# Kernel optimization log

Hardware: AMD Instinct MI355X
Metric: run time of the kernel (lower is better)

Reference implementation:

```python
import jax, jax.numpy as jnp
import numpy as np
from jax import lax

B, N, S, D1, D2 = 16, 4096, 1024, 128, 256
C_IN, C_MID, C_OUT = D1 + D2, 256, 128
BN_EPS = 1e-5


def setup_inputs() -> dict:
    key = jax.random.key(0)
    ks = jax.random.split(key, 12)
    return {
        "xyz1": jax.random.normal(ks[0], (B, N, 3), jnp.float32),
        "xyz2": jax.random.normal(ks[1], (B, S, 3), jnp.float32),
        "points1": jax.random.normal(ks[2], (B, N, D1), jnp.float32),
        "points2": jax.random.normal(ks[3], (B, S, D2), jnp.float32),
        # 1x1 Conv1d weights (kernel size 1 -> plain channel matmul)
        "W1": jax.random.normal(ks[4], (C_MID, C_IN), jnp.float32) * (1.0 / np.sqrt(C_IN)),
        "b1": jax.random.normal(ks[5], (C_MID,), jnp.float32) * 0.01,
        "g1": jnp.ones((C_MID,), jnp.float32),
        "be1": jnp.zeros((C_MID,), jnp.float32),
        "W2": jax.random.normal(ks[6], (C_OUT, C_MID), jnp.float32) * (1.0 / np.sqrt(C_MID)),
        "b2": jax.random.normal(ks[7], (C_OUT,), jnp.float32) * 0.01,
        "g2": jnp.ones((C_OUT,), jnp.float32),
        "be2": jnp.zeros((C_OUT,), jnp.float32),
    }


def _bn_relu(x, g, be):
    # BatchNorm1d in training mode: batch stats over (B, L) per channel, biased var
    mean = jnp.mean(x, axis=(0, 2), keepdims=True)
    var = jnp.var(x, axis=(0, 2), keepdims=True)
    y = (x - mean) * lax.rsqrt(var + BN_EPS)
    return jax.nn.relu(y * g[None, :, None] + be[None, :, None])


def reference(xyz1, xyz2, points1, points2, W1, b1, g1, be1, W2, b2, g2, be2):
    # squared pairwise distances [B,N,S] via ||a||^2 - 2ab + ||b||^2
    dist = (
        jnp.sum(xyz1 * xyz1, -1)[:, :, None]
        - 2.0 * jnp.einsum("bnd,bsd->bns", xyz1, xyz2)
        + jnp.sum(xyz2 * xyz2, -1)[:, None, :]
    )
    neg_d3, idx = lax.top_k(-dist, 3)            # 3 nearest neighbors
    d3 = -neg_d3                                  # [B,N,3]
    w = 1.0 / (d3 + 1e-8)
    w = w / jnp.sum(w, -1, keepdims=True)
    gathered = jax.vmap(lambda p, i: p[i])(points2, idx)   # [B,N,3,D2]
    interp = jnp.sum(gathered * w[..., None], axis=2)      # [B,N,D2]
    new_points = jnp.concatenate([points1, interp], axis=-1)  # [B,N,D1+D2]
    x = jnp.transpose(new_points, (0, 2, 1))                   # [B,C,N]
    x = _bn_relu(jnp.einsum("oc,bcn->bon", W1, x) + b1[None, :, None], g1, be1)
    x = _bn_relu(jnp.einsum("oc,bcn->bon", W2, x) + b2[None, :, None], g2, be2)
    return jnp.transpose(x, (0, 2, 1))                         # [B,N,C_OUT]
```

## Files before the change

### kernel.cpp

```cpp
#include <hip/hip_runtime.h>
#include <hip/hip_bf16.h>

#define NB    16
#define NPT   4096
#define NSRC  1024
#define ND1   128
#define ND2   256
#define NCIN  384
#define NCMID 256
#define NCOUT 128
#define BNTOT (NB * NPT)
#define BN_EPS 1e-5f

typedef float f32x4 __attribute__((ext_vector_type(4)));
typedef short bf16x8 __attribute__((ext_vector_type(8)));
typedef unsigned int uint;

union PK8 { unsigned short u[8]; uint4 q; };
union PK4 { unsigned short u[4]; uint2 q; };

static __device__ __forceinline__ unsigned short f2bf(float f) {
  __hip_bfloat16 h = __float2bfloat16(f);
  return __builtin_bit_cast(unsigned short, h);
}
static __device__ __forceinline__ float bf2f(unsigned short u) {
  return __builtin_bit_cast(float, (uint)u << 16);
}
static __device__ __forceinline__ void gl_lds16(const unsigned short* g, unsigned short* l) {
  __builtin_amdgcn_global_load_lds(
      (const __attribute__((address_space(1))) uint*)(const void*)g,
      (__attribute__((address_space(3))) uint*)(void*)l,
      16, 0, 0);
}

#if __has_builtin(__builtin_amdgcn_fmed3f)
#define MED3F(a, b, c) __builtin_amdgcn_fmed3f((a), (b), (c))
#else
#define MED3F(a, b, c) fmaxf((a), fminf((b), (c)))
#endif

static __device__ __forceinline__ bool prec(float da, int ia, float db, int ib) {
  return (da < db) || (da == db && ia < ib);
}

#define INSV(t0, t1, t2, j0, j1, j2, d, idx)                                   \
  {                                                                            \
    const bool c0 = (d) < t0;                                                  \
    const bool c1 = (d) < t1;                                                  \
    const bool c2 = (d) < t2;                                                  \
    const float m1 = MED3F(t0, t1, (d));                                       \
    const float m2 = fminf(t2, fmaxf(t1, (d)));                                \
    t0 = fminf(t0, (d));                                                       \
    j2 = c2 ? (c1 ? j1 : (idx)) : j2;                                          \
    j1 = c1 ? (c0 ? j0 : (idx)) : j1;                                          \
    j0 = c0 ? (idx) : j0;                                                      \
    t1 = m1; t2 = m2;                                                          \
  }

#define MERGE3(d0, j0, d1, j1, d2, j2, e0, i0, e1, i1, e2, i2)                 \
  {                                                                            \
    const bool p0 = prec(d0, j0, e0, i0);                                      \
    const float l0d = p0 ? e0 : d0; const int l0j = p0 ? i0 : j0;              \
    const float r0d = p0 ? d0 : e0; const int r0j = p0 ? j0 : i0;              \
    const bool p1 = prec(d1, j1, e1, i1);                                      \
    const float w1d = p1 ? d1 : e1; const int w1j = p1 ? j1 : i1;              \
    const bool pr1 = prec(l0d, l0j, w1d, w1j);                                 \
    const float r1d = pr1 ? l0d : w1d; const int r1j = pr1 ? l0j : w1j;        \
    const float q1d = pr1 ? w1d : l0d; const int q1j = pr1 ? w1j : l0j;        \
    const bool p2 = prec(d2, j2, e2, i2);                                      \
    const float w2d = p2 ? d2 : e2; const int w2j = p2 ? j2 : i2;              \
    const bool pr2 = prec(q1d, q1j, w2d, w2j);                                 \
    const float r2d = pr2 ? q1d : w2d; const int r2j = pr2 ? q1j : w2j;        \
    d0 = r0d; j0 = r0j; d1 = r1d; j1 = r1j; d2 = r2d; j2 = r2j;                \
  }

__global__ __launch_bounds__(256) void prep_w_kernel(
    const float* __restrict__ w1, const float* __restrict__ w2,
    unsigned short* __restrict__ w1b, unsigned short* __restrict__ w2b)
{
  const int i = blockIdx.x * 256 + threadIdx.x;
  const bool isW1 = i < 24576;
  const float4 v = isW1 ? ((const float4*)w1)[i] : ((const float4*)w2)[i - 24576];
  PK4 pk;
  pk.u[0] = f2bf(v.x); pk.u[1] = f2bf(v.y); pk.u[2] = f2bf(v.z); pk.u[3] = f2bf(v.w);
  if (isW1) ((uint2*)w1b)[i] = pk.q;
  else      ((uint2*)w2b)[i - 24576] = pk.q;
}

__global__ __launch_bounds__(512, 4) void fg1_kernel(
    const float* __restrict__ xyz1, const float* __restrict__ xyz2,
    const float* __restrict__ points1, const float* __restrict__ points2,
    const unsigned short* __restrict__ W1bf, const float* __restrict__ bias1,
    unsigned short* __restrict__ h1bf, float* __restrict__ sum1, float* __restrict__ sq1)
{
  __shared__ unsigned short sA[2][128][32];
  __shared__ unsigned short sB[2][256][32];
  __shared__ float4 s2t[4 * 257];
  __shared__ int   sj[128][3];
  __shared__ float sw[128][3];

  const int tid = threadIdx.x;
  const int lane = tid & 63;
  const int wave = tid >> 6;
  const int ptBase = blockIdx.x * 128;
  const int b = ptBase >> 12;

  const int fr = lane & 15;
  const int cs = lane >> 4;
  const int rdsh = ((cs ^ ((fr >> 1) & 3)) << 3);

  auto stageB = [&](int buf, int kt) {
    const int k0 = kt * 32;
#pragma unroll
    for (int c = 0; c < 2; ++c) {
      const int base = c * 512 + wave * 64;
      const int s = base + lane;
      const int row = s >> 2, c16 = s & 3;
      const int ks = c16 ^ ((row >> 1) & 3);
      gl_lds16(W1bf + (size_t)row * NCIN + k0 + ks * 8,
               &sB[buf][0][0] + base * 8);
    }
  };

  auto stageA = [&](int buf, int kt) {
    const int k0 = kt * 32;
    const int row = tid >> 2, c16 = tid & 3;
    const int ks = c16 ^ ((row >> 1) & 3);
    const int k = k0 + ks * 8;
    PK8 pk;
    if (k < ND1) {
      const float* src = points1 + (size_t)(ptBase + row) * ND1 + k;
      const float4 va = ((const float4*)src)[0];
      const float4 vb = ((const float4*)src)[1];
      pk.u[0] = f2bf(va.x); pk.u[1] = f2bf(va.y); pk.u[2] = f2bf(va.z); pk.u[3] = f2bf(va.w);
      pk.u[4] = f2bf(vb.x); pk.u[5] = f2bf(vb.y); pk.u[6] = f2bf(vb.z); pk.u[7] = f2bf(vb.w);
    } else {
      const float* p2 = points2 + (size_t)b * NSRC * ND2 + (k - ND1);
      const int j0 = sj[row][0], j1 = sj[row][1], j2 = sj[row][2];
      const float w0 = sw[row][0], w1 = sw[row][1], w2 = sw[row][2];
      const float4* r0 = (const float4*)(p2 + (size_t)j0 * ND2);
      const float4* r1 = (const float4*)(p2 + (size_t)j1 * ND2);
      const float4* r2 = (const float4*)(p2 + (size_t)j2 * ND2);
#pragma unroll
      for (int h = 0; h < 2; ++h) {
        const float4 va = r0[h], vb = r1[h], vc = r2[h];
        pk.u[h * 4 + 0] = f2bf(w0 * va.x + w1 * vb.x + w2 * vc.x);
        pk.u[h * 4 + 1] = f2bf(w0 * va.y + w1 * vb.y + w2 * vc.y);
        pk.u[h * 4 + 2] = f2bf(w0 * va.z + w1 * vb.z + w2 * vc.z);
        pk.u[h * 4 + 3] = f2bf(w0 * va.w + w1 * vb.w + w2 * vc.w);
      }
    }
    *(uint4*)(&sA[buf][0][0] + tid * 8) = pk.q;
  };

  stageB(0, 0);
  if (tid < 256) {
    const float* src = xyz2 + (size_t)b * NSRC * 3 + tid * 12;
    const float4 l0 = ((const float4*)src)[0];
    const float4 l1 = ((const float4*)src)[1];
    const float4 l2 = ((const float4*)src)[2];
    const float xs[4] = {l0.x, l0.w, l1.z, l2.y};
    const float ys[4] = {l0.y, l1.x, l1.w, l2.z};
    const float zs[4] = {l0.z, l1.y, l2.x, l2.w};
    const int qq = tid >> 6;
    const int ibase = (tid & 63) * 4;
#pragma unroll
    for (int u = 0; u < 4; ++u) {
      const float c = xs[u] * xs[u] + ys[u] * ys[u] + zs[u] * zs[u];
      float4 v;
      v.x = -2.0f * xs[u]; v.y = -2.0f * ys[u]; v.z = -2.0f * zs[u]; v.w = c;
      s2t[qq * 257 + ibase + u] = v;
    }
  }
  stageA(0, 0);
  __syncthreads();

  {
    const int ptl = tid >> 2;
    const int q = tid & 3;
    const int p = ptBase + ptl;
    const float ax = xyz1[(size_t)p * 3 + 0];
    const float ay = xyz1[(size_t)p * 3 + 1];
    const float az = xyz1[(size_t)p * 3 + 2];
    const float a2 = ax * ax + ay * ay + az * az;
    const float4* slab = &s2t[q * 257];
    const int qbase = q * 256;

    const float INF = 3.4e38f;
    float ta0 = INF, ta1 = INF, ta2 = INF; int ja0 = 0, ja1 = 0, ja2 = 0;
    float tb0 = INF, tb1 = INF, tb2 = INF; int jb0 = 0, jb1 = 0, jb2 = 0;

    for (int i = 0; i < 256; i += 2) {
      const float4 va = slab[i];
      float da = va.w + a2;
      da = fmaf(va.x, ax, da); da = fmaf(va.y, ay, da); da = fmaf(va.z, az, da);
      INSV(ta0, ta1, ta2, ja0, ja1, ja2, da, qbase + i);
      const float4 vb = slab[i + 1];
      float db = vb.w + a2;
      db = fmaf(vb.x, ax, db); db = fmaf(vb.y, ay, db); db = fmaf(vb.z, az, db);
      INSV(tb0, tb1, tb2, jb0, jb1, jb2, db, qbase + i + 1);
    }
    MERGE3(ta0, ja0, ta1, ja1, ta2, ja2, tb0, jb0, tb1, jb1, tb2, jb2);

#pragma unroll
    for (int m = 1; m <= 2; m <<= 1) {
      float e0 = __shfl_xor(ta0, m), e1 = __shfl_xor(ta1, m), e2 = __shfl_xor(ta2, m);
      int i0 = __shfl_xor(ja0, m), i1 = __shfl_xor(ja1, m), i2 = __shfl_xor(ja2, m);
      MERGE3(ta0, ja0, ta1, ja1, ta2, ja2, e0, i0, e1, i1, e2, i2);
    }

    if (q == 0) {
      float w0 = 1.f / (ta0 + 1e-8f), w1 = 1.f / (ta1 + 1e-8f), w2 = 1.f / (ta2 + 1e-8f);
      const float inv = 1.f / (w0 + w1 + w2);
      sj[ptl][0] = ja0; sj[ptl][1] = ja1; sj[ptl][2] = ja2;
      sw[ptl][0] = w0 * inv; sw[ptl][1] = w1 * inv; sw[ptl][2] = w2 * inv;
    }
  }
  __syncthreads();

  f32x4 acc[16];
#pragma unroll
  for (int j = 0; j < 16; ++j)
#pragma unroll
    for (int q = 0; q < 4; ++q) acc[j][q] = 0.0f;

  int cur = 0;
  for (int kt = 0; kt < 12; ++kt) {
    if (kt < 11) { stageB(cur ^ 1, kt + 1); stageA(cur ^ 1, kt + 1); }
    const bf16x8 a = *(const bf16x8*)&sA[cur][wave * 16 + fr][rdsh];
#pragma unroll
    for (int j = 0; j < 16; ++j) {
      const bf16x8 bv = *(const bf16x8*)&sB[cur][j * 16 + fr][rdsh];
      acc[j] = __builtin_amdgcn_mfma_f32_16x16x32_bf16(a, bv, acc[j], 0, 0, 0);
    }
    __syncthreads();
    cur ^= 1;
  }

  float* redS = (float*)&sA[0][0][0];
  float* redQ = redS + 2048;
  const int r0 = cs * 4;
#pragma unroll
  for (int j = 0; j < 16; ++j) {
    const int ch = j * 16 + fr;
    const float bb = bias1[ch];
    float s = 0.f, s2 = 0.f;
#pragma unroll
    for (int q = 0; q < 4; ++q) {
      const int pt = ptBase + wave * 16 + r0 + q;
      const float v = acc[j][q] + bb;
      h1bf[(size_t)pt * NCMID + ch] = f2bf(v);
      s += v; s2 += v * v;
    }
    s += __shfl_xor(s, 16);  s2 += __shfl_xor(s2, 16);
    s += __shfl_xor(s, 32);  s2 += __shfl_xor(s2, 32);
    if (cs == 0) { redS[wave * 256 + ch] = s; redQ[wave * 256 + ch] = s2; }
  }
  __syncthreads();
  if (tid < NCMID) {
    float s = 0.f, s2 = 0.f;
#pragma unroll
    for (int w = 0; w < 8; ++w) {
      s  += redS[w * 256 + tid];
      s2 += redQ[w * 256 + tid];
    }
    atomicAdd(&sum1[tid], s);
    atomicAdd(&sq1[tid], s2);
  }
}

template <int C>
__global__ void stats_kernel(const float* __restrict__ sum, const float* __restrict__ sumsq,
                             const float* __restrict__ g, const float* __restrict__ be,
                             float* __restrict__ a, float* __restrict__ d)
{
  const int c = threadIdx.x;
  const float mean = sum[c] * (1.0f / BNTOT);
  const float var = sumsq[c] * (1.0f / BNTOT) - mean * mean;
  const float inv = rsqrtf(var + BN_EPS);
  const float ac = g[c] * inv;
  a[c] = ac;
  d[c] = be[c] - mean * ac;
}

__global__ __launch_bounds__(256, 2) void gemm2_kernel(
    const unsigned short* __restrict__ h1bf, const unsigned short* __restrict__ W2bf,
    const float* __restrict__ bias2, const float* __restrict__ aff_a,
    const float* __restrict__ aff_d, unsigned short* __restrict__ h2bf,
    float* __restrict__ sum2, float* __restrict__ sq2)
{
  __shared__ unsigned short sA[2][128][32];
  __shared__ unsigned short sB[2][128][32];
  __shared__ float sa[NCMID], sd[NCMID];
  const int tid = threadIdx.x;
  const int lane = tid & 63;
  const int wave = tid >> 6;
  const int ptBase = blockIdx.x * 128;
  sa[tid] = aff_a[tid];
  sd[tid] = aff_d[tid];

  f32x4 acc[2][8];
#pragma unroll
  for (int m = 0; m < 2; ++m)
#pragma unroll
    for (int j = 0; j < 8; ++j)
#pragma unroll
      for (int q = 0; q < 4; ++q) acc[m][j][q] = 0.0f;

  const int fr = lane & 15;
  const int cs = lane >> 4;
  const int rdsh = ((cs ^ ((fr >> 1) & 3)) << 3);

  auto stageB = [&](int buf, int kt) {
    const int k0 = kt * 32;
#pragma unroll
    for (int c = 0; c < 2; ++c) {
      const int s = c * 256 + wave * 64 + lane;
      const int row = s >> 2, c16 = s & 3;
      const int ks = c16 ^ ((row >> 1) & 3);
      gl_lds16(W2bf + (size_t)row * NCMID + k0 + ks * 8,
               &sB[buf][0][0] + (c * 256 + wave * 64) * 8);
    }
  };
  auto stageA = [&](int buf, int kt) {
    const int k0 = kt * 32;
#pragma unroll
    for (int c = 0; c < 2; ++c) {
      const int s = c * 256 + tid;
      const int row = s >> 2, c16 = s & 3;
      const int ks = c16 ^ ((row >> 1) & 3);
      const int k = k0 + ks * 8;
      PK8 v;
      v.q = *(const uint4*)(h1bf + (size_t)(ptBase + row) * NCMID + k);
      PK8 pk;
#pragma unroll
      for (int j = 0; j < 8; ++j)
        pk.u[j] = f2bf(fmaxf(0.f, sa[k + j] * bf2f(v.u[j]) + sd[k + j]));
      *(uint4*)(&sA[buf][0][0] + s * 8) = pk.q;
    }
  };

  stageB(0, 0);
  __syncthreads();
  stageA(0, 0);
  __syncthreads();
  int cur = 0;
  for (int kt = 0; kt < 8; ++kt) {
    if (kt < 7) { stageB(cur ^ 1, kt + 1); stageA(cur ^ 1, kt + 1); }
    const bf16x8 a0 = *(const bf16x8*)&sA[cur][wave * 32 + fr][rdsh];
    const bf16x8 a1 = *(const bf16x8*)&sA[cur][wave * 32 + 16 + fr][rdsh];
#pragma unroll
    for (int j = 0; j < 8; ++j) {
      const bf16x8 b = *(const bf16x8*)&sB[cur][j * 16 + fr][rdsh];
      acc[0][j] = __builtin_amdgcn_mfma_f32_16x16x32_bf16(a0, b, acc[0][j], 0, 0, 0);
      acc[1][j] = __builtin_amdgcn_mfma_f32_16x16x32_bf16(a1, b, acc[1][j], 0, 0, 0);
    }
    __syncthreads();
    cur ^= 1;
  }

  float* redS = (float*)&sA[0][0][0];
  float* redQ = redS + 512;
  const int col = fr;
  const int r0 = cs * 4;
#pragma unroll
  for (int j = 0; j < 8; ++j) {
    const int ch = j * 16 + col;
    const float bb = bias2[ch];
    float s = 0.f, s2 = 0.f;
#pragma unroll
    for (int m = 0; m < 2; ++m)
#pragma unroll
      for (int q = 0; q < 4; ++q) {
        const int pt = ptBase + wave * 32 + m * 16 + r0 + q;
        const float v = acc[m][j][q] + bb;
        h2bf[(size_t)pt * NCOUT + ch] = f2bf(v);
        s += v; s2 += v * v;
      }
    s += __shfl_xor(s, 16);  s2 += __shfl_xor(s2, 16);
    s += __shfl_xor(s, 32);  s2 += __shfl_xor(s2, 32);
    if (cs == 0) { redS[wave * 128 + fr * 8 + j] = s; redQ[wave * 128 + fr * 8 + j] = s2; }
  }
  __syncthreads();
  if (tid < NCOUT) {
    const int ch = tid;
    const int f = ch & 15, j = ch >> 4;
    float s = 0.f, s2 = 0.f;
#pragma unroll
    for (int w = 0; w < 4; ++w) {
      s  += redS[w * 128 + f * 8 + j];
      s2 += redQ[w * 128 + f * 8 + j];
    }
    atomicAdd(&sum2[ch], s);
    atomicAdd(&sq2[ch], s2);
  }
}

__global__ __launch_bounds__(256) void final_kernel(
    const unsigned short* __restrict__ h2bf, float* __restrict__ out,
    const float* __restrict__ a2, const float* __restrict__ d2)
{
  __shared__ float sa[NCOUT], sd[NCOUT];
  if (threadIdx.x < NCOUT) { sa[threadIdx.x] = a2[threadIdx.x]; sd[threadIdx.x] = d2[threadIdx.x]; }
  __syncthreads();
  const int total8 = BNTOT * NCOUT / 8;
  for (int i = blockIdx.x * blockDim.x + threadIdx.x; i < total8;
       i += gridDim.x * blockDim.x) {
    PK8 v; v.q = ((const uint4*)h2bf)[i];
    const int c = (i & 15) * 8;
    float4 o0, o1;
    o0.x = fmaxf(0.f, sa[c + 0] * bf2f(v.u[0]) + sd[c + 0]);
    o0.y = fmaxf(0.f, sa[c + 1] * bf2f(v.u[1]) + sd[c + 1]);
    o0.z = fmaxf(0.f, sa[c + 2] * bf2f(v.u[2]) + sd[c + 2]);
    o0.w = fmaxf(0.f, sa[c + 3] * bf2f(v.u[3]) + sd[c + 3]);
    o1.x = fmaxf(0.f, sa[c + 4] * bf2f(v.u[4]) + sd[c + 4]);
    o1.y = fmaxf(0.f, sa[c + 5] * bf2f(v.u[5]) + sd[c + 5]);
    o1.z = fmaxf(0.f, sa[c + 6] * bf2f(v.u[6]) + sd[c + 6]);
    o1.w = fmaxf(0.f, sa[c + 7] * bf2f(v.u[7]) + sd[c + 7]);
    ((float4*)out)[i * 2]     = o0;
    ((float4*)out)[i * 2 + 1] = o1;
  }
}

extern "C" void kernel_launch(void* const* d_in, const int* in_sizes, int n_in,
                              void* d_out, int out_size, void* d_ws, size_t ws_size,
                              hipStream_t stream) {
  const float* xyz1    = (const float*)d_in[0];
  const float* xyz2    = (const float*)d_in[1];
  const float* points1 = (const float*)d_in[2];
  const float* points2 = (const float*)d_in[3];
  const float* W1      = (const float*)d_in[4];
  const float* b1      = (const float*)d_in[5];
  const float* g1      = (const float*)d_in[6];
  const float* be1     = (const float*)d_in[7];
  const float* W2      = (const float*)d_in[8];
  const float* b2      = (const float*)d_in[9];
  const float* g2      = (const float*)d_in[10];
  const float* be2     = (const float*)d_in[11];
  float* out = (float*)d_out;

  char* ws = (char*)d_ws;
  const size_t h1_bytes  = (size_t)BNTOT * NCMID * 2;
  const size_t h2_bytes  = (size_t)BNTOT * NCOUT * 2;
  const size_t w1b_bytes = (size_t)NCMID * NCIN * 2;
  const size_t w2b_bytes = (size_t)NCOUT * NCMID * 2;
  unsigned short* h1bf = (unsigned short*)ws;
  unsigned short* h2bf = (unsigned short*)(ws + h1_bytes);
  unsigned short* W1bf = (unsigned short*)(ws + h1_bytes + h2_bytes);
  unsigned short* W2bf = (unsigned short*)(ws + h1_bytes + h2_bytes + w1b_bytes);
  float* stats = (float*)(ws + h1_bytes + h2_bytes + w1b_bytes + w2b_bytes);
  float* sum1 = stats;
  float* sq1  = stats + 256;
  float* sum2 = stats + 512;
  float* sq2  = stats + 640;
  float* a1   = stats + 768;
  float* dd1  = stats + 1024;
  float* a2v  = stats + 1280;
  float* dd2v = stats + 1408;

  hipMemsetAsync(stats, 0, 768 * sizeof(float), stream);

  prep_w_kernel<<<128, 256, 0, stream>>>(W1, W2, W1bf, W2bf);
  fg1_kernel<<<BNTOT / 128, 512, 0, stream>>>(xyz1, xyz2, points1, points2,
                                              W1bf, b1, h1bf, sum1, sq1);
  stats_kernel<NCMID><<<1, NCMID, 0, stream>>>(sum1, sq1, g1, be1, a1, dd1);
  gemm2_kernel<<<BNTOT / 128, 256, 0, stream>>>(h1bf, W2bf, b2, a1, dd1, h2bf, sum2, sq2);
  stats_kernel<NCOUT><<<1, NCOUT, 0, stream>>>(sum2, sq2, g2, be2, a2v, dd2v);
  final_kernel<<<2048, 256, 0, stream>>>(h2bf, out, a2v, dd2v);
}
```

Baseline: 124.5 us.

## Drop LDS staging in fg1, load GEMM fragments directly from global memory

The fused gather+GEMM1 kernel now uses 64-point blocks of 256 threads. Each wave builds its A fragment directly in registers, from points1 or the interpolated points2 rows, and reads W1 bf16 fragments straight from global/L2 instead of double-buffered LDS tiles. This removes the per-k-step barriers and LDS traffic. BN1 statistics are written as per-block partials and reduced by a new colred kernel instead of per-block atomics. The trade-off is more redundant global/L2 reads of W1 per block, with no software pipelining of the loads, plus one extra kernel launch.

```diff
diff --git a/kernel.cpp b/kernel.cpp
--- a/kernel.cpp
+++ b/kernel.cpp
@@ -87,74 +87,25 @@
   else      ((uint2*)w2b)[i - 24576] = pk.q;
 }
 
-__global__ __launch_bounds__(512, 4) void fg1_kernel(
+__global__ __launch_bounds__(256, 3) void fg1_kernel(
     const float* __restrict__ xyz1, const float* __restrict__ xyz2,
     const float* __restrict__ points1, const float* __restrict__ points2,
     const unsigned short* __restrict__ W1bf, const float* __restrict__ bias1,
-    unsigned short* __restrict__ h1bf, float* __restrict__ sum1, float* __restrict__ sq1)
-{
-  __shared__ unsigned short sA[2][128][32];
-  __shared__ unsigned short sB[2][256][32];
+    unsigned short* __restrict__ h1bf, float* __restrict__ pS, float* __restrict__ pQ)
+{
   __shared__ float4 s2t[4 * 257];
-  __shared__ int   sj[128][3];
-  __shared__ float sw[128][3];
+  __shared__ int   sj[64][3];
+  __shared__ float sw[64][3];
+  __shared__ float redS[4][256];
+  __shared__ float redQ[4][256];
 
   const int tid = threadIdx.x;
   const int lane = tid & 63;
   const int wave = tid >> 6;
-  const int ptBase = blockIdx.x * 128;
+  const int ptBase = blockIdx.x * 64;
   const int b = ptBase >> 12;
 
-  const int fr = lane & 15;
-  const int cs = lane >> 4;
-  const int rdsh = ((cs ^ ((fr >> 1) & 3)) << 3);
-
-  auto stageB = [&](int buf, int kt) {
-    const int k0 = kt * 32;
-#pragma unroll
-    for (int c = 0; c < 2; ++c) {
-      const int base = c * 512 + wave * 64;
-      const int s = base + lane;
-      const int row = s >> 2, c16 = s & 3;
-      const int ks = c16 ^ ((row >> 1) & 3);
-      gl_lds16(W1bf + (size_t)row * NCIN + k0 + ks * 8,
-               &sB[buf][0][0] + base * 8);
-    }
-  };
-
-  auto stageA = [&](int buf, int kt) {
-    const int k0 = kt * 32;
-    const int row = tid >> 2, c16 = tid & 3;
-    const int ks = c16 ^ ((row >> 1) & 3);
-    const int k = k0 + ks * 8;
-    PK8 pk;
-    if (k < ND1) {
-      const float* src = points1 + (size_t)(ptBase + row) * ND1 + k;
-      const float4 va = ((const float4*)src)[0];
-      const float4 vb = ((const float4*)src)[1];
-      pk.u[0] = f2bf(va.x); pk.u[1] = f2bf(va.y); pk.u[2] = f2bf(va.z); pk.u[3] = f2bf(va.w);
-      pk.u[4] = f2bf(vb.x); pk.u[5] = f2bf(vb.y); pk.u[6] = f2bf(vb.z); pk.u[7] = f2bf(vb.w);
-    } else {
-      const float* p2 = points2 + (size_t)b * NSRC * ND2 + (k - ND1);
-      const int j0 = sj[row][0], j1 = sj[row][1], j2 = sj[row][2];
-      const float w0 = sw[row][0], w1 = sw[row][1], w2 = sw[row][2];
-      const float4* r0 = (const float4*)(p2 + (size_t)j0 * ND2);
-      const float4* r1 = (const float4*)(p2 + (size_t)j1 * ND2);
-      const float4* r2 = (const float4*)(p2 + (size_t)j2 * ND2);
-#pragma unroll
-      for (int h = 0; h < 2; ++h) {
-        const float4 va = r0[h], vb = r1[h], vc = r2[h];
-        pk.u[h * 4 + 0] = f2bf(w0 * va.x + w1 * vb.x + w2 * vc.x);
-        pk.u[h * 4 + 1] = f2bf(w0 * va.y + w1 * vb.y + w2 * vc.y);
-        pk.u[h * 4 + 2] = f2bf(w0 * va.z + w1 * vb.z + w2 * vc.z);
-        pk.u[h * 4 + 3] = f2bf(w0 * va.w + w1 * vb.w + w2 * vc.w);
-      }
-    }
-    *(uint4*)(&sA[buf][0][0] + tid * 8) = pk.q;
-  };
-
-  stageB(0, 0);
-  if (tid < 256) {
+  {
     const float* src = xyz2 + (size_t)b * NSRC * 3 + tid * 12;
     const float4 l0 = ((const float4*)src)[0];
     const float4 l1 = ((const float4*)src)[1];
@@ -172,12 +123,11 @@
       s2t[qq * 257 + ibase + u] = v;
     }
   }
-  stageA(0, 0);
   __syncthreads();
 
   {
-    const int ptl = tid >> 2;
-    const int q = tid & 3;
+    const int ptl = wave * 16 + (lane >> 2);
+    const int q = lane & 3;
     const int p = ptBase + ptl;
     const float ax = xyz1[(size_t)p * 3 + 0];
     const float ay = xyz1[(size_t)p * 3 + 1];
@@ -216,7 +166,18 @@
       sw[ptl][0] = w0 * inv; sw[ptl][1] = w1 * inv; sw[ptl][2] = w2 * inv;
     }
   }
-  __syncthreads();
+
+  const int fr = lane & 15;
+  const int cs = lane >> 4;
+  const int wrow = wave * 16 + fr;
+  const int pA = ptBase + wrow;
+
+  const int gj0 = sj[wrow][0], gj1 = sj[wrow][1], gj2 = sj[wrow][2];
+  const float gw0 = sw[wrow][0], gw1 = sw[wrow][1], gw2 = sw[wrow][2];
+  const float* p2base = points2 + (size_t)b * NSRC * ND2;
+  const float* r0p = p2base + (size_t)gj0 * ND2;
+  const float* r1p = p2base + (size_t)gj1 * ND2;
+  const float* r2p = p2base + (size_t)gj2 * ND2;
 
   f32x4 acc[16];
 #pragma unroll
@@ -224,21 +185,46 @@
 #pragma unroll
     for (int q = 0; q < 4; ++q) acc[j][q] = 0.0f;
 
-  int cur = 0;
   for (int kt = 0; kt < 12; ++kt) {
-    if (kt < 11) { stageB(cur ^ 1, kt + 1); stageA(cur ^ 1, kt + 1); }
-    const bf16x8 a = *(const bf16x8*)&sA[cur][wave * 16 + fr][rdsh];
-#pragma unroll
-    for (int j = 0; j < 16; ++j) {
-      const bf16x8 bv = *(const bf16x8*)&sB[cur][j * 16 + fr][rdsh];
-      acc[j] = __builtin_amdgcn_mfma_f32_16x16x32_bf16(a, bv, acc[j], 0, 0, 0);
-    }
-    __syncthreads();
-    cur ^= 1;
-  }
-
-  float* redS = (float*)&sA[0][0][0];
-  float* redQ = redS + 2048;
+    const int k = kt * 32 + cs * 8;
+    PK8 af;
+    if (kt < 4) {
+      const float* src = points1 + (size_t)pA * ND1 + k;
+      const float4 va = ((const float4*)src)[0];
+      const float4 vb = ((const float4*)src)[1];
+      af.u[0] = f2bf(va.x); af.u[1] = f2bf(va.y); af.u[2] = f2bf(va.z); af.u[3] = f2bf(va.w);
+      af.u[4] = f2bf(vb.x); af.u[5] = f2bf(vb.y); af.u[6] = f2bf(vb.z); af.u[7] = f2bf(vb.w);
+    } else {
+      const int ko = k - ND1;
+      const float4* g0 = (const float4*)(r0p + ko);
+      const float4* g1 = (const float4*)(r1p + ko);
+      const float4* g2 = (const float4*)(r2p + ko);
+#pragma unroll
+      for (int h = 0; h < 2; ++h) {
+        const float4 va = g0[h], vb = g1[h], vc = g2[h];
+        af.u[h * 4 + 0] = f2bf(gw0 * va.x + gw1 * vb.x + gw2 * vc.x);
+        af.u[h * 4 + 1] = f2bf(gw0 * va.y + gw1 * vb.y + gw2 * vc.y);
+        af.u[h * 4 + 2] = f2bf(gw0 * va.z + gw1 * vb.z + gw2 * vc.z);
+        af.u[h * 4 + 3] = f2bf(gw0 * va.w + gw1 * vb.w + gw2 * vc.w);
+      }
+    }
+    const bf16x8 a = __builtin_bit_cast(bf16x8, af.q);
+#pragma unroll
+    for (int g = 0; g < 2; ++g) {
+      uint4 bq[8];
+#pragma unroll
+      for (int jj = 0; jj < 8; ++jj) {
+        const int j = g * 8 + jj;
+        bq[jj] = *(const uint4*)(W1bf + (size_t)(j * 16 + fr) * NCIN + k);
+      }
+#pragma unroll
+      for (int jj = 0; jj < 8; ++jj) {
+        const bf16x8 bv = __builtin_bit_cast(bf16x8, bq[jj]);
+        acc[g * 8 + jj] = __builtin_amdgcn_mfma_f32_16x16x32_bf16(a, bv, acc[g * 8 + jj], 0, 0, 0);
+      }
+    }
+  }
+
   const int r0 = cs * 4;
 #pragma unroll
   for (int j = 0; j < 16; ++j) {
@@ -254,19 +240,31 @@
     }
     s += __shfl_xor(s, 16);  s2 += __shfl_xor(s2, 16);
     s += __shfl_xor(s, 32);  s2 += __shfl_xor(s2, 32);
-    if (cs == 0) { redS[wave * 256 + ch] = s; redQ[wave * 256 + ch] = s2; }
-  }
-  __syncthreads();
-  if (tid < NCMID) {
-    float s = 0.f, s2 = 0.f;
-#pragma unroll
-    for (int w = 0; w < 8; ++w) {
-      s  += redS[w * 256 + tid];
-      s2 += redQ[w * 256 + tid];
-    }
-    atomicAdd(&sum1[tid], s);
-    atomicAdd(&sq1[tid], s2);
-  }
+    if (cs == 0) { redS[wave][ch] = s; redQ[wave][ch] = s2; }
+  }
+  __syncthreads();
+  {
+    const int ch = tid;
+    const float s  = redS[0][ch] + redS[1][ch] + redS[2][ch] + redS[3][ch];
+    const float s2 = redQ[0][ch] + redQ[1][ch] + redQ[2][ch] + redQ[3][ch];
+    pS[(size_t)blockIdx.x * NCMID + ch] = s;
+    pQ[(size_t)blockIdx.x * NCMID + ch] = s2;
+  }
+}
+
+__global__ __launch_bounds__(256) void colred_kernel(
+    const float* __restrict__ pS, const float* __restrict__ pQ,
+    float* __restrict__ sum1, float* __restrict__ sq1)
+{
+  const int ch = threadIdx.x;
+  const int r0 = blockIdx.x * 32;
+  float s = 0.f, s2 = 0.f;
+  for (int i = 0; i < 32; ++i) {
+    s  += pS[(size_t)(r0 + i) * NCMID + ch];
+    s2 += pQ[(size_t)(r0 + i) * NCMID + ch];
+  }
+  atomicAdd(&sum1[ch], s);
+  atomicAdd(&sq1[ch], s2);
 }
 
 template <int C>
@@ -444,11 +442,14 @@
   const size_t h2_bytes  = (size_t)BNTOT * NCOUT * 2;
   const size_t w1b_bytes = (size_t)NCMID * NCIN * 2;
   const size_t w2b_bytes = (size_t)NCOUT * NCMID * 2;
+  const size_t ps_bytes  = (size_t)1024 * NCMID * 4;
   unsigned short* h1bf = (unsigned short*)ws;
   unsigned short* h2bf = (unsigned short*)(ws + h1_bytes);
   unsigned short* W1bf = (unsigned short*)(ws + h1_bytes + h2_bytes);
   unsigned short* W2bf = (unsigned short*)(ws + h1_bytes + h2_bytes + w1b_bytes);
-  float* stats = (float*)(ws + h1_bytes + h2_bytes + w1b_bytes + w2b_bytes);
+  float* pS = (float*)(ws + h1_bytes + h2_bytes + w1b_bytes + w2b_bytes);
+  float* pQ = (float*)(ws + h1_bytes + h2_bytes + w1b_bytes + w2b_bytes + ps_bytes);
+  float* stats = (float*)(ws + h1_bytes + h2_bytes + w1b_bytes + w2b_bytes + 2 * ps_bytes);
   float* sum1 = stats;
   float* sq1  = stats + 256;
   float* sum2 = stats + 512;
@@ -461,8 +462,9 @@
   hipMemsetAsync(stats, 0, 768 * sizeof(float), stream);
 
   prep_w_kernel<<<128, 256, 0, stream>>>(W1, W2, W1bf, W2bf);
-  fg1_kernel<<<BNTOT / 128, 512, 0, stream>>>(xyz1, xyz2, points1, points2,
-                                              W1bf, b1, h1bf, sum1, sq1);
+  fg1_kernel<<<BNTOT / 64, 256, 0, stream>>>(xyz1, xyz2, points1, points2,
+                                             W1bf, b1, h1bf, pS, pQ);
+  colred_kernel<<<32, 256, 0, stream>>>(pS, pQ, sum1, sq1);
   stats_kernel<NCMID><<<1, NCMID, 0, stream>>>(sum1, sq1, g1, be1, a1, dd1);
   gemm2_kernel<<<BNTOT / 128, 256, 0, stream>>>(h1bf, W2bf, b2, a1, dd1, h2bf, sum2, sq2);
   stats_kernel<NCOUT><<<1, NCOUT, 0, stream>>>(sum2, sq2, g2, be2, a2v, dd2v);
```

After: 214.6 us. +72.4%, slower.

## Interleave KNN search with first GEMM k-tiles and swizzle block order

Applied to the files above, without the earlier changes.

Moves the 3-NN search into the first three iterations of the points1 GEMM loop, so the distance scan overlaps with MFMA work on the points1 channels, which do not need neighbor indices. Each thread keeps its own neighbor indices and weights in registers after the 4-lane shuffle merge, and gathers points2 rows directly instead of going through shared sj/sw arrays. This removes one barrier and the serial KNN phase before the GEMM. It also remaps blockIdx so consecutive blocks come from different batches, which spreads the load differently across the chip. The cost is higher register pressure, since the KNN state stays live during the MFMA loop.

```diff
diff --git a/kernel.cpp b/kernel.cpp
--- a/kernel.cpp
+++ b/kernel.cpp
@@ -74,6 +74,18 @@
     d0 = r0d; j0 = r0j; d1 = r1d; j1 = r1j; d2 = r2d; j2 = r2j;                \
   }
 
+#define KNN_PAIR(i)                                                            \
+  {                                                                            \
+    const float4 va = n_slab[(i)];                                             \
+    float da = va.w + n_a2;                                                    \
+    da = fmaf(va.x, n_ax, da); da = fmaf(va.y, n_ay, da); da = fmaf(va.z, n_az, da); \
+    INSV(n_ta0, n_ta1, n_ta2, n_ja0, n_ja1, n_ja2, da, n_qbase + (i));         \
+    const float4 vb = n_slab[(i) + 1];                                         \
+    float db = vb.w + n_a2;                                                    \
+    db = fmaf(vb.x, n_ax, db); db = fmaf(vb.y, n_ay, db); db = fmaf(vb.z, n_az, db); \
+    INSV(n_tb0, n_tb1, n_tb2, n_jb0, n_jb1, n_jb2, db, n_qbase + (i) + 1);     \
+  }
+
 __global__ __launch_bounds__(256) void prep_w_kernel(
     const float* __restrict__ w1, const float* __restrict__ w2,
     unsigned short* __restrict__ w1b, unsigned short* __restrict__ w2b)
@@ -96,13 +108,13 @@
   __shared__ unsigned short sA[2][128][32];
   __shared__ unsigned short sB[2][256][32];
   __shared__ float4 s2t[4 * 257];
-  __shared__ int   sj[128][3];
-  __shared__ float sw[128][3];
 
   const int tid = threadIdx.x;
   const int lane = tid & 63;
   const int wave = tid >> 6;
-  const int ptBase = blockIdx.x * 128;
+
+  const int bid = (int)(blockIdx.x & 7) * 64 + (int)(blockIdx.x >> 3);
+  const int ptBase = bid * 128;
   const int b = ptBase >> 12;
 
   const int fr = lane & 15;
@@ -122,11 +134,15 @@
     }
   };
 
+  const float* g0p = points2;
+  const float* g1p = points2;
+  const float* g2p = points2;
+  float gw0 = 0.f, gw1 = 0.f, gw2 = 0.f;
+
   auto stageA = [&](int buf, int kt) {
-    const int k0 = kt * 32;
     const int row = tid >> 2, c16 = tid & 3;
     const int ks = c16 ^ ((row >> 1) & 3);
-    const int k = k0 + ks * 8;
+    const int k = kt * 32 + ks * 8;
     PK8 pk;
     if (k < ND1) {
       const float* src = points1 + (size_t)(ptBase + row) * ND1 + k;
@@ -135,23 +151,33 @@
       pk.u[0] = f2bf(va.x); pk.u[1] = f2bf(va.y); pk.u[2] = f2bf(va.z); pk.u[3] = f2bf(va.w);
       pk.u[4] = f2bf(vb.x); pk.u[5] = f2bf(vb.y); pk.u[6] = f2bf(vb.z); pk.u[7] = f2bf(vb.w);
     } else {
-      const float* p2 = points2 + (size_t)b * NSRC * ND2 + (k - ND1);
-      const int j0 = sj[row][0], j1 = sj[row][1], j2 = sj[row][2];
-      const float w0 = sw[row][0], w1 = sw[row][1], w2 = sw[row][2];
-      const float4* r0 = (const float4*)(p2 + (size_t)j0 * ND2);
-      const float4* r1 = (const float4*)(p2 + (size_t)j1 * ND2);
-      const float4* r2 = (const float4*)(p2 + (size_t)j2 * ND2);
+      const int ko = k - ND1;
+      const float4* r0 = (const float4*)(g0p + ko);
+      const float4* r1 = (const float4*)(g1p + ko);
+      const float4* r2 = (const float4*)(g2p + ko);
 #pragma unroll
       for (int h = 0; h < 2; ++h) {
         const float4 va = r0[h], vb = r1[h], vc = r2[h];
-        pk.u[h * 4 + 0] = f2bf(w0 * va.x + w1 * vb.x + w2 * vc.x);
-        pk.u[h * 4 + 1] = f2bf(w0 * va.y + w1 * vb.y + w2 * vc.y);
-        pk.u[h * 4 + 2] = f2bf(w0 * va.z + w1 * vb.z + w2 * vc.z);
-        pk.u[h * 4 + 3] = f2bf(w0 * va.w + w1 * vb.w + w2 * vc.w);
+        pk.u[h * 4 + 0] = f2bf(gw0 * va.x + gw1 * vb.x + gw2 * vc.x);
+        pk.u[h * 4 + 1] = f2bf(gw0 * va.y + gw1 * vb.y + gw2 * vc.y);
+        pk.u[h * 4 + 2] = f2bf(gw0 * va.z + gw1 * vb.z + gw2 * vc.z);
+        pk.u[h * 4 + 3] = f2bf(gw0 * va.w + gw1 * vb.w + gw2 * vc.w);
       }
     }
     *(uint4*)(&sA[buf][0][0] + tid * 8) = pk.q;
   };
+
+  const int ptl = tid >> 2;
+  const float n_ax = xyz1[(size_t)(ptBase + ptl) * 3 + 0];
+  const float n_ay = xyz1[(size_t)(ptBase + ptl) * 3 + 1];
+  const float n_az = xyz1[(size_t)(ptBase + ptl) * 3 + 2];
+  const float n_a2 = n_ax * n_ax + n_ay * n_ay + n_az * n_az;
+  const float4* n_slab = &s2t[(tid & 3) * 257];
+  const int n_qbase = (tid & 3) * 256;
+  const float INF = 3.4e38f;
+  float n_ta0 = INF, n_ta1 = INF, n_ta2 = INF;
+  float n_tb0 = INF, n_tb1 = INF, n_tb2 = INF;
+  int n_ja0 = 0, n_ja1 = 0, n_ja2 = 0, n_jb0 = 0, n_jb1 = 0, n_jb2 = 0;
 
   stageB(0, 0);
   if (tid < 256) {
@@ -175,66 +201,45 @@
   stageA(0, 0);
   __syncthreads();
 
-  {
-    const int ptl = tid >> 2;
-    const int q = tid & 3;
-    const int p = ptBase + ptl;
-    const float ax = xyz1[(size_t)p * 3 + 0];
-    const float ay = xyz1[(size_t)p * 3 + 1];
-    const float az = xyz1[(size_t)p * 3 + 2];
-    const float a2 = ax * ax + ay * ay + az * az;
-    const float4* slab = &s2t[q * 257];
-    const int qbase = q * 256;
-
-    const float INF = 3.4e38f;
-    float ta0 = INF, ta1 = INF, ta2 = INF; int ja0 = 0, ja1 = 0, ja2 = 0;
-    float tb0 = INF, tb1 = INF, tb2 = INF; int jb0 = 0, jb1 = 0, jb2 = 0;
-
-    for (int i = 0; i < 256; i += 2) {
-      const float4 va = slab[i];
-      float da = va.w + a2;
-      da = fmaf(va.x, ax, da); da = fmaf(va.y, ay, da); da = fmaf(va.z, az, da);
-      INSV(ta0, ta1, ta2, ja0, ja1, ja2, da, qbase + i);
-      const float4 vb = slab[i + 1];
-      float db = vb.w + a2;
-      db = fmaf(vb.x, ax, db); db = fmaf(vb.y, ay, db); db = fmaf(vb.z, az, db);
-      INSV(tb0, tb1, tb2, jb0, jb1, jb2, db, qbase + i + 1);
-    }
-    MERGE3(ta0, ja0, ta1, ja1, ta2, ja2, tb0, jb0, tb1, jb1, tb2, jb2);
-
-#pragma unroll
-    for (int m = 1; m <= 2; m <<= 1) {
-      float e0 = __shfl_xor(ta0, m), e1 = __shfl_xor(ta1, m), e2 = __shfl_xor(ta2, m);
-      int i0 = __shfl_xor(ja0, m), i1 = __shfl_xor(ja1, m), i2 = __shfl_xor(ja2, m);
-      MERGE3(ta0, ja0, ta1, ja1, ta2, ja2, e0, i0, e1, i1, e2, i2);
-    }
-
-    if (q == 0) {
-      float w0 = 1.f / (ta0 + 1e-8f), w1 = 1.f / (ta1 + 1e-8f), w2 = 1.f / (ta2 + 1e-8f);
+  f32x4 acc[16];
+#pragma unroll
+  for (int j = 0; j < 16; ++j)
+#pragma unroll
+    for (int q = 0; q < 4; ++q) acc[j][q] = 0.0f;
+
+  int ki = 0;
+  int buf = 0;
+  for (int kt = 0; kt < 12; ++kt) {
+    if (kt < 11) stageB(buf ^ 1, kt + 1);
+    if (kt < 3) {
+      const int take = (kt < 2) ? 43 : 42;
+      for (int u = 0; u < take; ++u, ++ki) KNN_PAIR(2 * ki);
+    } else if (kt == 3) {
+      MERGE3(n_ta0, n_ja0, n_ta1, n_ja1, n_ta2, n_ja2,
+             n_tb0, n_jb0, n_tb1, n_jb1, n_tb2, n_jb2);
+#pragma unroll
+      for (int m = 1; m <= 2; m <<= 1) {
+        float e0 = __shfl_xor(n_ta0, m), e1 = __shfl_xor(n_ta1, m), e2 = __shfl_xor(n_ta2, m);
+        int i0 = __shfl_xor(n_ja0, m), i1 = __shfl_xor(n_ja1, m), i2 = __shfl_xor(n_ja2, m);
+        MERGE3(n_ta0, n_ja0, n_ta1, n_ja1, n_ta2, n_ja2, e0, i0, e1, i1, e2, i2);
+      }
+      float w0 = 1.f / (n_ta0 + 1e-8f), w1 = 1.f / (n_ta1 + 1e-8f), w2 = 1.f / (n_ta2 + 1e-8f);
       const float inv = 1.f / (w0 + w1 + w2);
-      sj[ptl][0] = ja0; sj[ptl][1] = ja1; sj[ptl][2] = ja2;
-      sw[ptl][0] = w0 * inv; sw[ptl][1] = w1 * inv; sw[ptl][2] = w2 * inv;
-    }
-  }
-  __syncthreads();
-
-  f32x4 acc[16];
-#pragma unroll
-  for (int j = 0; j < 16; ++j)
-#pragma unroll
-    for (int q = 0; q < 4; ++q) acc[j][q] = 0.0f;
-
-  int cur = 0;
-  for (int kt = 0; kt < 12; ++kt) {
-    if (kt < 11) { stageB(cur ^ 1, kt + 1); stageA(cur ^ 1, kt + 1); }
-    const bf16x8 a = *(const bf16x8*)&sA[cur][wave * 16 + fr][rdsh];
+      gw0 = w0 * inv; gw1 = w1 * inv; gw2 = w2 * inv;
+      const float* p2base = points2 + (size_t)b * NSRC * ND2;
+      g0p = p2base + (size_t)n_ja0 * ND2;
+      g1p = p2base + (size_t)n_ja1 * ND2;
+      g2p = p2base + (size_t)n_ja2 * ND2;
+    }
+    if (kt < 11) stageA(buf ^ 1, kt + 1);
+    const bf16x8 a = *(const bf16x8*)&sA[buf][wave * 16 + fr][rdsh];
 #pragma unroll
     for (int j = 0; j < 16; ++j) {
-      const bf16x8 bv = *(const bf16x8*)&sB[cur][j * 16 + fr][rdsh];
+      const bf16x8 bv = *(const bf16x8*)&sB[buf][j * 16 + fr][rdsh];
       acc[j] = __builtin_amdgcn_mfma_f32_16x16x32_bf16(a, bv, acc[j], 0, 0, 0);
     }
     __syncthreads();
-    cur ^= 1;
+    buf ^= 1;
   }
 
   float* redS = (float*)&sA[0][0][0];
```

Result: slower. 130.6 us (+4.8%).
